# Kernel optimization log

Measured on AMD Instinct MI355X. Metric: run time of the kernel, lower is better.

## Reference

```python
import jax, jax.numpy as jnp
import numpy as np

T, B, D, H = 64, 512, 512, 2048


def setup_inputs() -> dict:
    key = jax.random.key(0)
    ks = jax.random.split(key, 6)
    y0 = jax.random.normal(ks[0], (B, D), dtype=jnp.float32)
    # strictly increasing per-sample time grids with small dt for stability
    dt = jax.random.uniform(ks[1], (T, B), dtype=jnp.float32) * 0.01 + 0.001
    t = jnp.cumsum(dt, axis=0)
    W1 = jax.random.normal(ks[2], (D, H), dtype=jnp.float32) * (1.0 / np.sqrt(D))
    b1 = jnp.zeros((H,), dtype=jnp.float32)
    W2 = jax.random.normal(ks[3], (H, D), dtype=jnp.float32) * (1.0 / np.sqrt(H))
    b2 = jnp.zeros((D,), dtype=jnp.float32)
    return {"y0": y0, "t": t, "W1": W1, "b1": b1, "W2": W2, "b2": b2}


def reference(y0, t, W1, b1, W2, b2):
    # func(t, y): autonomous 2-layer tanh MLP (t unused, as in common NeuralODE funcs)
    def f(y):
        return jnp.tanh(y @ W1 + b1) @ W2 + b2

    def step(y, dt):  # y: [B, D], dt: [B]
        dtb = dt[:, None]
        k1 = dtb * f(y)
        k2 = dtb * f(y + k1 * 0.5)
        k3 = dtb * f(y + k2 * 0.5)
        k4 = dtb * f(y + k3)
        y_new = y + (k1 + 2.0 * k2 + 2.0 * k3 + k4) / 6.0
        return y_new, y_new

    dts = t[1:] - t[:-1]  # [T-1, B] per-sample step sizes
    _, ys = jax.lax.scan(step, y0, dts)
    return jnp.concatenate([y0[None], ys], axis=0)  # [T, B, D]
```

## Files before the change

kernel.cpp:

```cpp
#include <hip/hip_runtime.h>

#define Tn 64
#define Bn 512
#define Dn 512
#define Hn 2048

typedef __attribute__((ext_vector_type(8))) short s16x8;
typedef __attribute__((ext_vector_type(4))) float f32x4;
typedef __attribute__((ext_vector_type(4))) unsigned int u32x4;
typedef unsigned int u32;
typedef unsigned long long u64;
typedef unsigned short u16;

__device__ __forceinline__ u16 f2bf(float f) {
    u32 u = __builtin_bit_cast(u32, f);
    return (u16)((u + 0x7fffu + ((u >> 16) & 1u)) >> 16);
}
__device__ __forceinline__ float bf2f(u32 v) {
    return __builtin_bit_cast(float, v << 16);
}
__device__ __forceinline__ float tanh_fast(float x) {
    float e = __builtin_amdgcn_exp2f(x * 2.885390081777927f);
    return 1.0f - 2.0f * __builtin_amdgcn_rcpf(e + 1.0f);
}
__device__ __forceinline__ u32 agent_ld(const u32* p) {
    return __hip_atomic_load((u32*)p, __ATOMIC_RELAXED, __HIP_MEMORY_SCOPE_AGENT);
}
__device__ __forceinline__ void agent_st(u32* p, u32 v) {
    __hip_atomic_store(p, v, __ATOMIC_RELAXED, __HIP_MEMORY_SCOPE_AGENT);
}
__device__ __forceinline__ u32 get_xcc() {
    u32 x;
    asm volatile("s_getreg_b32 %0, hwreg(HW_REG_XCC_ID)" : "=s"(x));
    return x & 0xffu;
}

template<bool XL>
__device__ __forceinline__ void eld128(u32x4& d, u32 vo, const void* base) {
    if constexpr (XL)
        asm volatile("global_load_dwordx4 %0, %1, %2 sc0"
                     : "=v"(d) : "v"(vo), "s"(base) : "memory");
    else
        asm volatile("global_load_dwordx4 %0, %1, %2 sc0 sc1 nt"
                     : "=v"(d) : "v"(vo), "s"(base) : "memory");
}
template<bool XL>
__device__ __forceinline__ void eld32(u32& d, u32 vo, const void* base) {
    if constexpr (XL)
        asm volatile("global_load_dword %0, %1, %2 sc0"
                     : "=v"(d) : "v"(vo), "s"(base) : "memory");
    else
        asm volatile("global_load_dword %0, %1, %2 sc0 sc1 nt"
                     : "=v"(d) : "v"(vo), "s"(base) : "memory");
}
template<bool XL>
__device__ __forceinline__ void est64(void* pa, u64 v) {
    if constexpr (XL)
        asm volatile("global_store_dwordx2 %0, %1, off sc0" :: "v"(pa), "v"(v) : "memory");
    else
        asm volatile("global_store_dwordx2 %0, %1, off sc0 sc1" :: "v"(pa), "v"(v) : "memory");
}
template<bool XL>
__device__ __forceinline__ void est32(void* pa, u32 v) {
    if constexpr (XL)
        asm volatile("global_store_dword %0, %1, off sc0" :: "v"(pa), "v"(v) : "memory");
    else
        asm volatile("global_store_dword %0, %1, off sc0 sc1" :: "v"(pa), "v"(v) : "memory");
}

__global__ void pack_w(const float* __restrict__ W1, const float* __restrict__ W2,
                       u16* __restrict__ w1p, u16* __restrict__ w2p) {
    const int i = blockIdx.x * 256 + threadIdx.x;
    const int e = i & 7;
    const int lane = (i >> 3) & 63;
    const int krem = ((lane >> 4) << 3) + e;
    const int ncol = lane & 15;
    {
        const int kt = (i >> 9) & 15, nt = i >> 13;
        const int k = (kt << 5) + krem, n = (nt << 4) + ncol;
        w1p[i] = f2bf(W1[k * Hn + n]);
    }
    {
        const int kt = (i >> 9) & 63, nt = i >> 15;
        const int k = (kt << 5) + krem, n = (nt << 4) + ncol;
        w2p[i] = f2bf(W2[k * Dn + n]);
    }
}


template<bool XL>
__device__ __forceinline__ void stage_a(const u32* ybrC, char* ldsA, int tid) {
    u32x4 d0, d1;
    const u32 vo = (u32)(tid << 5);
    eld128<XL>(d0, vo, ybrC);
    eld128<XL>(d1, vo + 16u, ybrC);
    asm volatile("s_waitcnt vmcnt(0)" : "+v"(d0), "+v"(d1) :: "memory");
    const u32 row = (u32)(tid >> 5);
    const u32 dst = vo ^ ((row & 7u) << 4);
    *(u32x4*)(ldsA + dst) = d0;
    *(u32x4*)(ldsA + (dst ^ 16u)) = d1;
}

__device__ __forceinline__ void stage_a0(const float* y0, int c, char* ldsA, int tid) {
    const float4* yc = (const float4*)(y0 + (size_t)(c << 4) * Dn);
    #pragma unroll
    for (int it = 0; it < 4; ++it) {
        const int idx = (it << 9) + tid;
        const float4 v = yc[idx];
        const u32 row = (u32)idx >> 7;
        u64 pk = (u64)((u32)f2bf(v.x) | ((u32)f2bf(v.y) << 16)) |
                 ((u64)((u32)f2bf(v.z) | ((u32)f2bf(v.w) << 16)) << 32);
        const u32 dst = (row * 1024u + ((u32)(idx & 127) << 3)) ^ ((row & 7u) << 4);
        *(u64*)(ldsA + dst) = pk;
    }
}

__device__ __forceinline__ void gemm1(const char* ldsA, char* ldsH,
                                      const s16x8 (&w1r)[16], float bia,
                                      u32 abase, u32 aswz, int w, int l15, int kg) {
    f32x4 g1 = f32x4{bia, bia, bia, bia};
    #pragma unroll
    for (int kt = 0; kt < 16; ++kt) {
        const s16x8 a = *(const s16x8*)(ldsA + ((abase + ((u32)kt << 6)) ^ aswz));
        g1 = __builtin_amdgcn_mfma_f32_16x16x32_bf16(a, w1r[kt], g1, 0, 0, 0);
    }
    #pragma unroll
    for (int j = 0; j < 4; ++j) {
        const u32 row = (u32)((kg << 2) + j);
        const u32 bo = (row * 256u + (((u32)(w << 4) + (u32)l15) << 1)) ^ ((row & 7u) << 4);
        *(u16*)(ldsH + bo) = f2bf(tanh_fast(g1[j]));
    }
}

template<bool XL>
__device__ __forceinline__ void gemm2_store(const char* ldsH, char* kpC,
                                            const s16x8 (&w2r)[4][4],
                                            u32 hbase, u32 aswz, int w, int l15,
                                            int kg, int h) {
    f32x4 acc[4];
    #pragma unroll
    for (int c = 0; c < 4; ++c) acc[c] = f32x4{0.f, 0.f, 0.f, 0.f};
    #pragma unroll
    for (int ks2 = 0; ks2 < 4; ++ks2) {
        const s16x8 ha = *(const s16x8*)(ldsH + ((hbase + ((u32)ks2 << 6)) ^ aswz));
        #pragma unroll
        for (int c = 0; c < 4; ++c)
            acc[c] = __builtin_amdgcn_mfma_f32_16x16x32_bf16(ha, w2r[c][ks2], acc[c], 0, 0, 0);
    }
    #pragma unroll
    for (int c = 0; c < 4; ++c) {
        const int nt = (w << 2) + c;
        const int o = nt >> 1;
        const int sc2 = ((nt & 1) << 4) + l15;
        u64 pk = (u64)((u32)f2bf(acc[c][0]) | ((u32)f2bf(acc[c][1]) << 16)) |
                 ((u64)((u32)f2bf(acc[c][2]) | ((u32)f2bf(acc[c][3]) << 16)) << 32);
        void* pa = kpC + (size_t)((o << 4) + h) * 1024 + (u32)((sc2 << 5) + (kg << 3));
        est64<XL>(pa, pk);
    }
}

template<bool XL>
__device__ __forceinline__ void owner_phase(int s, float& ys, float& ks, float& dtv,
                                            int brow, const char* kpC, u32* ybrC,
                                            const float* tt, float* out, float b2c,
                                            int colg, int sc, int rm, int h, int tid) {
    float sacc = 0.f;
    {
        const u32 bo = ((u32)h << 14) + (u32)((sc << 5) + ((rm >> 1) << 2));
        u32 t0,t1,t2,t3,t4,t5,t6,t7,t8,t9,ta,tb,tc,td,te,tf;
        eld32<XL>(t0, bo + (0u << 10), kpC);  eld32<XL>(t1, bo + (1u << 10), kpC);
        eld32<XL>(t2, bo + (2u << 10), kpC);  eld32<XL>(t3, bo + (3u << 10), kpC);
        eld32<XL>(t4, bo + (4u << 10), kpC);  eld32<XL>(t5, bo + (5u << 10), kpC);
        eld32<XL>(t6, bo + (6u << 10), kpC);  eld32<XL>(t7, bo + (7u << 10), kpC);
        eld32<XL>(t8, bo + (8u << 10), kpC);  eld32<XL>(t9, bo + (9u << 10), kpC);
        eld32<XL>(ta, bo + (10u << 10), kpC); eld32<XL>(tb, bo + (11u << 10), kpC);
        eld32<XL>(tc, bo + (12u << 10), kpC); eld32<XL>(td, bo + (13u << 10), kpC);
        eld32<XL>(te, bo + (14u << 10), kpC); eld32<XL>(tf, bo + (15u << 10), kpC);
        asm volatile("s_waitcnt vmcnt(0)"
                     : "+v"(t0),"+v"(t1),"+v"(t2),"+v"(t3),
                       "+v"(t4),"+v"(t5),"+v"(t6),"+v"(t7),
                       "+v"(t8),"+v"(t9),"+v"(ta),"+v"(tb),
                       "+v"(tc),"+v"(td),"+v"(te),"+v"(tf) :: "memory");
        const bool hi = (rm & 1);
#define ACC1(d) sacc += bf2f(hi ? ((d) >> 16) : ((d) & 0xffffu))
        ACC1(t0); ACC1(t1); ACC1(t2); ACC1(t3);
        ACC1(t4); ACC1(t5); ACC1(t6); ACC1(t7);
        ACC1(t8); ACC1(t9); ACC1(ta); ACC1(tb);
        ACC1(tc); ACC1(td); ACC1(te); ACC1(tf);
#undef ACC1
    }
    const int step = s >> 2, sub = s & 3;
    if (sub == 0)
        dtv = tt[(step + 1) * Bn + brow] - tt[step * Bn + brow];
    const float kk = dtv * (sacc + b2c);
    float yin;
    if (sub == 0)      { ks = kk;         yin = ys + 0.5f * kk; }
    else if (sub == 1) { ks += 2.f * kk;  yin = ys + 0.5f * kk; }
    else if (sub == 2) { ks += 2.f * kk;  yin = ys + kk; }
    else {
        ks += kk; ys += ks * (1.f / 6.f); yin = ys;
        __builtin_nontemporal_store(ys, &out[((step + 1) * Bn + brow) * Dn + colg]);
    }
    if (s < 251) {
        const u32 my = (u32)f2bf(yin);
        const u32 pu = (u32)__shfl_xor((int)my, 16, 64);
        if ((sc & 1) == 0) {
            u32* ba = ybrC + (rm << 8) + (h << 4) + (sc >> 1);
            est32<XL>(ba, my | (pu << 16));
        }
    }
}

template<bool XL>
__device__ __forceinline__ void ode_loop(
    const float* y0, const float* tt, float* out,
    char* A0, char* A1, char* H0, char* H1,
    const s16x8 (&w1r)[16], const s16x8 (&w2r)[4][4],
    float bia, float b2c, u32 abase, u32 aswz, u32 hbase,
    u32* ybr0, u32* ybr1, char* kp0, char* kp1,
    u32* fl1c0, u32* fl1c1, u32* fl2c0, u32* fl2c1,
    int c0, int c1, int brow0, int brow1, int colg,
    int tid, int w, int l15, int kg, int sc, int rm, int h,
    float ys0, float ys1) {
    float ks0 = 0.f, ks1 = 0.f, dt0 = 0.f, dt1 = 0.f;
    #pragma unroll 1
    for (int s = 0; s < 252; ++s) {
        if (s == 0) {
            stage_a0(y0, c0, A0, tid);
            stage_a0(y0, c1, A1, tid);
        } else {
            if (tid < 32) {
                u32* f = (tid < 16) ? (fl2c0 + tid) : (fl2c1 + (tid & 15));
                while (agent_ld(f) < (u32)s) __builtin_amdgcn_s_sleep(1);
            }
            __syncthreads();
            stage_a<XL>(ybr0, A0, tid);
            stage_a<XL>(ybr1, A1, tid);
        }
        __syncthreads();
        gemm1(A0, H0, w1r, bia, abase, aswz, w, l15, kg);
        gemm1(A1, H1, w1r, bia, abase, aswz, w, l15, kg);
        __syncthreads();
        gemm2_store<XL>(H0, kp0, w2r, hbase, aswz, w, l15, kg, h);
        gemm2_store<XL>(H1, kp1, w2r, hbase, aswz, w, l15, kg, h);
        asm volatile("s_waitcnt vmcnt(0)" ::: "memory");
        __syncthreads();
        if (tid == 0) {
            agent_st(fl1c0 + h, (u32)(s + 1));
            agent_st(fl1c1 + h, (u32)(s + 1));
        }
        if (tid < 32) {
            u32* f = (tid < 16) ? (fl1c0 + tid) : (fl1c1 + (tid & 15));
            while (agent_ld(f) < (u32)(s + 1)) __builtin_amdgcn_s_sleep(1);
        }
        __syncthreads();
        owner_phase<XL>(s, ys0, ks0, dt0, brow0, kp0, ybr0,
                        tt, out, b2c, colg, sc, rm, h, tid);
        owner_phase<XL>(s, ys1, ks1, dt1, brow1, kp1, ybr1,
                        tt, out, b2c, colg, sc, rm, h, tid);
        if (s < 251) {
            asm volatile("s_waitcnt vmcnt(0)" ::: "memory");
            __syncthreads();
            if (tid == 0) {
                agent_st(fl2c0 + h, (u32)(s + 1));
                agent_st(fl2c1 + h, (u32)(s + 1));
            }
        }
    }
}

__launch_bounds__(512, 2)
__global__ void ode_v12(const float* __restrict__ y0, const float* __restrict__ tt,
                        const float* __restrict__ b1, const float* __restrict__ b2,
                        const u16* __restrict__ w1p, const u16* __restrict__ w2p,
                        float* __restrict__ out, u16* __restrict__ ybuf,
                        u16* __restrict__ kpart, u32* __restrict__ flags1,
                        u32* __restrict__ flags2, u32* __restrict__ xslot,
                        u32* __restrict__ xmode) {
    __shared__ u16 lds_A0[16 * 512], lds_A1[16 * 512];
    __shared__ u16 lds_H0[16 * 128], lds_H1[16 * 128];
    __shared__ u32 smode;
    char* A0 = (char*)lds_A0; char* A1 = (char*)lds_A1;
    char* H0 = (char*)lds_H0; char* H1 = (char*)lds_H1;

    const int tid = threadIdx.x;
    const int w = tid >> 6, lane = tid & 63, l15 = lane & 15, kg = lane >> 4;
    const int p = blockIdx.x & 15, h = blockIdx.x >> 4;
    const int c0 = p << 1, c1 = c0 + 1;

    if (tid == 0) {
        agent_st(xslot + (p << 4) + h, get_xcc() + 1u);
        if (h == 0) {
            u32 ref = 0; bool same = true;
            #pragma unroll 1
            for (int i = 0; i < 16; ++i) {
                u32 v;
                while ((v = agent_ld(xslot + (p << 4) + i)) == 0u)
                    __builtin_amdgcn_s_sleep(1);
                if (i == 0) ref = v; else same = same && (v == ref);
            }
            agent_st(xmode + p, same ? 1u : 2u);
        }
        u32 m;
        while ((m = agent_ld(xmode + p)) == 0u) __builtin_amdgcn_s_sleep(1);
        smode = m;
    }

    const int sc = tid >> 4, rm = tid & 15;
    const int colg = (h << 5) + sc;
    const int brow0 = (c0 << 4) + rm, brow1 = (c1 << 4) + rm;
    const float b2c = b2[colg];
    float ys0 = y0[brow0 * Dn + colg];
    float ys1 = y0[brow1 * Dn + colg];
    __builtin_nontemporal_store(ys0, &out[brow0 * Dn + colg]);
    __builtin_nontemporal_store(ys1, &out[brow1 * Dn + colg]);

    s16x8 w1r[16];
    #pragma unroll
    for (int kt = 0; kt < 16; ++kt)
        w1r[kt] = *(const s16x8*)&w1p[((size_t)((h << 3) + w) * 16 + kt) * 512 + (lane << 3)];
    s16x8 w2r[4][4];
    #pragma unroll
    for (int cc = 0; cc < 4; ++cc)
        #pragma unroll
        for (int ks2 = 0; ks2 < 4; ++ks2)
            w2r[cc][ks2] = *(const s16x8*)&w2p[((size_t)((w << 2) + cc) * 64 + (h << 2) + ks2) * 512 + (lane << 3)];
    const float bia = b1[(h << 7) + (w << 4) + l15];

    const u32 abase = (u32)l15 * 1024u + ((u32)kg << 4);
    const u32 aswz = ((u32)(l15 & 7)) << 4;
    const u32 hbase = (u32)l15 * 256u + ((u32)kg << 4);

    u32* ybr0 = (u32*)(ybuf + (size_t)c0 * 16 * 512);
    u32* ybr1 = (u32*)(ybuf + (size_t)c1 * 16 * 512);
    char* kp0 = (char*)kpart + (size_t)c0 * (256 * 1024);
    char* kp1 = (char*)kpart + (size_t)c1 * (256 * 1024);
    u32* fl1c0 = flags1 + (c0 << 4); u32* fl1c1 = flags1 + (c1 << 4);
    u32* fl2c0 = flags2 + (c0 << 4); u32* fl2c1 = flags2 + (c1 << 4);

    __syncthreads();
    const u32 mode = smode;

    if (mode == 1u)
        ode_loop<true>(y0, tt, out, A0, A1, H0, H1, w1r, w2r, bia, b2c,
                       abase, aswz, hbase, ybr0, ybr1, kp0, kp1,
                       fl1c0, fl1c1, fl2c0, fl2c1, c0, c1, brow0, brow1, colg,
                       tid, w, l15, kg, sc, rm, h, ys0, ys1);
    else
        ode_loop<false>(y0, tt, out, A0, A1, H0, H1, w1r, w2r, bia, b2c,
                        abase, aswz, hbase, ybr0, ybr1, kp0, kp1,
                        fl1c0, fl1c1, fl2c0, fl2c1, c0, c1, brow0, brow1, colg,
                        tid, w, l15, kg, sc, rm, h, ys0, ys1);
}

__launch_bounds__(512, 2)
__global__ void ode_rk4_fb(const float* __restrict__ y0, const float* __restrict__ tt,
                           const float* __restrict__ b1, const float* __restrict__ b2,
                           const u16* __restrict__ w1p, const u16* __restrict__ w2p,
                           float* __restrict__ out) {
    __shared__ u16 lds_ys[16 * Dn];
    __shared__ u16 lds_hid[16 * Hn];
    __shared__ float lds_dt[16];
    const int tid = threadIdx.x;
    const int w = tid >> 6, lane = tid & 63, l15 = lane & 15, kgrp = lane >> 4;
    const int row0 = blockIdx.x << 4;
    float yreg[4][4], ksum[4][4], kk[4][4];
    float b1v[16], b2v[4], dtv[4];
    #pragma unroll
    for (int nt = 0; nt < 16; ++nt) b1v[nt] = b1[(w << 8) + (nt << 4) + l15];
    #pragma unroll
    for (int c = 0; c < 4; ++c) b2v[c] = b2[(w << 6) + (c << 4) + l15];
    #pragma unroll
    for (int c = 0; c < 4; ++c)
        #pragma unroll
        for (int j = 0; j < 4; ++j) {
            const int rr = (kgrp << 2) + j;
            const int col = (w << 6) + (c << 4) + l15;
            const float v = y0[(row0 + rr) * Dn + col];
            yreg[c][j] = v; ksum[c][j] = 0.f; kk[c][j] = 0.f;
            out[(row0 + rr) * Dn + col] = v;
        }
    const u16* wv1 = w1p + ((w << 4) * (16 * 512)) + (lane << 3);
    const u16* wv2 = w2p + ((w << 2) * (64 * 512)) + (lane << 3);
    const int arow = l15;
    const unsigned swzA = (unsigned)((arow & 7) << 3);
    for (int step = 0; step < Tn - 1; ++step) {
        if (tid < 16)
            lds_dt[tid] = tt[(step + 1) * Bn + row0 + tid] - tt[step * Bn + row0 + tid];
        #pragma unroll 1
        for (int s = 0; s < 4; ++s) {
            const float ci = (s == 3) ? 1.0f : ((s == 0) ? 0.0f : 0.5f);
            #pragma unroll
            for (int c = 0; c < 4; ++c)
                #pragma unroll
                for (int j = 0; j < 4; ++j) {
                    const int rr = (kgrp << 2) + j;
                    const int col = (w << 6) + (c << 4) + l15;
                    lds_ys[(unsigned)((rr << 9) + col) ^ (unsigned)((rr & 7) << 3)] =
                        f2bf(yreg[c][j] + ci * kk[c][j]);
                }
            __syncthreads();
            if (s == 0) {
                #pragma unroll
                for (int j = 0; j < 4; ++j) dtv[j] = lds_dt[(kgrp << 2) + j];
            }
            f32x4 acc[16];
            #pragma unroll
            for (int nt = 0; nt < 16; ++nt)
                #pragma unroll
                for (int j = 0; j < 4; ++j) acc[nt][j] = b1v[nt];
            #pragma unroll 2
            for (int kt = 0; kt < 16; ++kt) {
                const unsigned ia = ((unsigned)((arow << 9) + (kt << 5) + (kgrp << 3))) ^ swzA;
                const s16x8 a = *(const s16x8*)&lds_ys[ia];
                #pragma unroll
                for (int nt = 0; nt < 16; ++nt) {
                    const s16x8 bfrag = *(const s16x8*)&wv1[nt * 8192 + kt * 512];
                    acc[nt] = __builtin_amdgcn_mfma_f32_16x16x32_bf16(a, bfrag, acc[nt], 0, 0, 0);
                }
            }
            #pragma unroll
            for (int nt = 0; nt < 16; ++nt)
                #pragma unroll
                for (int j = 0; j < 4; ++j) {
                    const int rr = (kgrp << 2) + j;
                    const int col = (w << 8) + (nt << 4) + l15;
                    lds_hid[(unsigned)((rr << 11) + col) ^ (unsigned)((rr & 7) << 3)] =
                        f2bf(tanh_fast(acc[nt][j]));
                }
            __syncthreads();
            f32x4 acc2[4];
            #pragma unroll
            for (int c = 0; c < 4; ++c)
                #pragma unroll
                for (int j = 0; j < 4; ++j) acc2[c][j] = 0.f;
            #pragma unroll 2
            for (int kt = 0; kt < 64; ++kt) {
                const unsigned ia = ((unsigned)((arow << 11) + (kt << 5) + (kgrp << 3))) ^ swzA;
                const s16x8 a = *(const s16x8*)&lds_hid[ia];
                #pragma unroll
                for (int c = 0; c < 4; ++c) {
                    const s16x8 bfrag = *(const s16x8*)&wv2[c * 32768 + kt * 512];
                    acc2[c] = __builtin_amdgcn_mfma_f32_16x16x32_bf16(a, bfrag, acc2[c], 0, 0, 0);
                }
            }
            const float wq = (s == 0 || s == 3) ? 1.0f : 2.0f;
            #pragma unroll
            for (int c = 0; c < 4; ++c)
                #pragma unroll
                for (int j = 0; j < 4; ++j) {
                    const float kv = dtv[j] * (acc2[c][j] + b2v[c]);
                    kk[c][j] = kv;
                    ksum[c][j] = (s == 0) ? kv : ksum[c][j] + wq * kv;
                }
        }
        #pragma unroll
        for (int c = 0; c < 4; ++c)
            #pragma unroll
            for (int j = 0; j < 4; ++j) {
                const int rr = (kgrp << 2) + j;
                const int col = (w << 6) + (c << 4) + l15;
                yreg[c][j] += ksum[c][j] * (1.0f / 6.0f);
                out[((step + 1) * Bn + row0 + rr) * Dn + col] = yreg[c][j];
            }
    }
}

extern "C" void kernel_launch(void* const* d_in, const int* in_sizes, int n_in,
                              void* d_out, int out_size, void* d_ws, size_t ws_size,
                              hipStream_t stream) {
    const float* y0 = (const float*)d_in[0];
    const float* tt = (const float*)d_in[1];
    const float* W1 = (const float*)d_in[2];
    const float* b1 = (const float*)d_in[3];
    const float* W2 = (const float*)d_in[4];
    const float* b2 = (const float*)d_in[5];
    float* out = (float*)d_out;
    char* ws = (char*)d_ws;

    const size_t sz_fl = (size_t)64 * 1024;
    const size_t sz_x = 4096;
    const size_t sz_w = (size_t)Dn * Hn * 2;
    const size_t sz_ybuf = (size_t)32 * 16 * 512 * 2;
    const size_t sz_kpart = (size_t)32 * 16 * 16 * 1024;
    const size_t needed = 2 * sz_fl + sz_x + 2 * sz_w + sz_ybuf + sz_kpart + 4096;

    u32* flags1 = (u32*)ws;
    u32* flags2 = (u32*)(ws + sz_fl);
    u32* xslot = (u32*)(ws + 2 * sz_fl);
    u32* xmode = (u32*)(ws + 2 * sz_fl + 1024);
    u16* w1p = (u16*)(ws + 2 * sz_fl + sz_x);
    u16* w2p = (u16*)(ws + 2 * sz_fl + sz_x + sz_w);
    u16* ybuf = (u16*)(ws + 2 * sz_fl + sz_x + 2 * sz_w);
    u16* kpart = (u16*)(ws + 2 * sz_fl + sz_x + 2 * sz_w + sz_ybuf);

    if (ws_size >= needed) {
        hipMemsetAsync(ws, 0, 2 * sz_fl + sz_x, stream);
        pack_w<<<4096, 256, 0, stream>>>(W1, W2, w1p, w2p);
        void* args[] = {&y0, &tt, &b1, &b2, &w1p, &w2p, &out, &ybuf, &kpart,
                        &flags1, &flags2, &xslot, &xmode};
        hipLaunchCooperativeKernel((void*)ode_v12, dim3(256), dim3(512), args, 0, stream);
    } else {
        u16* f1 = (u16*)ws;
        u16* f2 = f1 + (size_t)Dn * Hn;
        pack_w<<<4096, 256, 0, stream>>>(W1, W2, f1, f2);
        ode_rk4_fb<<<32, 512, 0, stream>>>(y0, tt, b1, b2, f1, f2, out);
    }
}
```

Baseline: 1.859 ms.

## Repartition cooperative RK4 kernel: one batch chunk per block, 8 hidden-slice blocks

The cooperative ODE kernel changes from 16 chunk-pairs × 16 hidden-slice blocks to 32 chunks × 8 hidden-slice blocks. Each block now handles a single 16-row batch chunk with double the W1/W2 register slice, so each group synchronizes across 8 blocks instead of 16. This is meant to shrink the per-substep flag fan-in and the partial-sum reduction, which now reads 8 partials instead of 16. In exchange each block holds twice the weight registers, so launch bounds drop to 1 block per CU and register pressure rises.

```diff
diff --git a/kernel.cpp b/kernel.cpp
--- a/kernel.cpp
+++ b/kernel.cpp
@@ -36,22 +36,22 @@
 }
 
 template<bool XL>
-__device__ __forceinline__ void eld128(u32x4& d, u32 vo, const void* base) {
+__device__ __forceinline__ void eld128p(u32x4& d, const void* p) {
     if constexpr (XL)
-        asm volatile("global_load_dwordx4 %0, %1, %2 sc0"
-                     : "=v"(d) : "v"(vo), "s"(base) : "memory");
+        asm volatile("global_load_dwordx4 %0, %1, off sc0"
+                     : "=v"(d) : "v"(p) : "memory");
     else
-        asm volatile("global_load_dwordx4 %0, %1, %2 sc0 sc1 nt"
-                     : "=v"(d) : "v"(vo), "s"(base) : "memory");
-}
-template<bool XL>
-__device__ __forceinline__ void eld32(u32& d, u32 vo, const void* base) {
+        asm volatile("global_load_dwordx4 %0, %1, off sc0 sc1 nt"
+                     : "=v"(d) : "v"(p) : "memory");
+}
+template<bool XL>
+__device__ __forceinline__ void eld32p(u32& d, const void* p) {
     if constexpr (XL)
-        asm volatile("global_load_dword %0, %1, %2 sc0"
-                     : "=v"(d) : "v"(vo), "s"(base) : "memory");
+        asm volatile("global_load_dword %0, %1, off sc0"
+                     : "=v"(d) : "v"(p) : "memory");
     else
-        asm volatile("global_load_dword %0, %1, %2 sc0 sc1 nt"
-                     : "=v"(d) : "v"(vo), "s"(base) : "memory");
+        asm volatile("global_load_dword %0, %1, off sc0 sc1 nt"
+                     : "=v"(d) : "v"(p) : "memory");
 }
 template<bool XL>
 __device__ __forceinline__ void est64(void* pa, u64 v) {
@@ -89,12 +89,13 @@
 
 
 template<bool XL>
-__device__ __forceinline__ void stage_a(const u32* ybrC, char* ldsA, int tid) {
+__device__ __forceinline__ void stage_a(const char* ybrC, char* ldsA, int tid) {
     u32x4 d0, d1;
+    const char* src = ybrC + ((u32)tid << 5);
+    eld128p<XL>(d0, src);
+    eld128p<XL>(d1, src + 16);
+    asm volatile("s_waitcnt vmcnt(0)" : "+v"(d0), "+v"(d1) :: "memory");
     const u32 vo = (u32)(tid << 5);
-    eld128<XL>(d0, vo, ybrC);
-    eld128<XL>(d1, vo + 16u, ybrC);
-    asm volatile("s_waitcnt vmcnt(0)" : "+v"(d0), "+v"(d1) :: "memory");
     const u32 row = (u32)(tid >> 5);
     const u32 dst = vo ^ ((row & 7u) << 4);
     *(u32x4*)(ldsA + dst) = d0;
@@ -115,242 +116,226 @@
     }
 }
 
-__device__ __forceinline__ void gemm1(const char* ldsA, char* ldsH,
-                                      const s16x8 (&w1r)[16], float bia,
-                                      u32 abase, u32 aswz, int w, int l15, int kg) {
-    f32x4 g1 = f32x4{bia, bia, bia, bia};
-    #pragma unroll
-    for (int kt = 0; kt < 16; ++kt) {
-        const s16x8 a = *(const s16x8*)(ldsA + ((abase + ((u32)kt << 6)) ^ aswz));
-        g1 = __builtin_amdgcn_mfma_f32_16x16x32_bf16(a, w1r[kt], g1, 0, 0, 0);
-    }
-    #pragma unroll
-    for (int j = 0; j < 4; ++j) {
-        const u32 row = (u32)((kg << 2) + j);
-        const u32 bo = (row * 256u + (((u32)(w << 4) + (u32)l15) << 1)) ^ ((row & 7u) << 4);
-        *(u16*)(ldsH + bo) = f2bf(tanh_fast(g1[j]));
-    }
-}
-
-template<bool XL>
-__device__ __forceinline__ void gemm2_store(const char* ldsH, char* kpC,
-                                            const s16x8 (&w2r)[4][4],
-                                            u32 hbase, u32 aswz, int w, int l15,
-                                            int kg, int h) {
-    f32x4 acc[4];
-    #pragma unroll
-    for (int c = 0; c < 4; ++c) acc[c] = f32x4{0.f, 0.f, 0.f, 0.f};
-    #pragma unroll
-    for (int ks2 = 0; ks2 < 4; ++ks2) {
-        const s16x8 ha = *(const s16x8*)(ldsH + ((hbase + ((u32)ks2 << 6)) ^ aswz));
-        #pragma unroll
-        for (int c = 0; c < 4; ++c)
-            acc[c] = __builtin_amdgcn_mfma_f32_16x16x32_bf16(ha, w2r[c][ks2], acc[c], 0, 0, 0);
-    }
-    #pragma unroll
-    for (int c = 0; c < 4; ++c) {
-        const int nt = (w << 2) + c;
-        const int o = nt >> 1;
-        const int sc2 = ((nt & 1) << 4) + l15;
-        u64 pk = (u64)((u32)f2bf(acc[c][0]) | ((u32)f2bf(acc[c][1]) << 16)) |
-                 ((u64)((u32)f2bf(acc[c][2]) | ((u32)f2bf(acc[c][3]) << 16)) << 32);
-        void* pa = kpC + (size_t)((o << 4) + h) * 1024 + (u32)((sc2 << 5) + (kg << 3));
-        est64<XL>(pa, pk);
-    }
-}
-
-template<bool XL>
-__device__ __forceinline__ void owner_phase(int s, float& ys, float& ks, float& dtv,
-                                            int brow, const char* kpC, u32* ybrC,
-                                            const float* tt, float* out, float b2c,
-                                            int colg, int sc, int rm, int h, int tid) {
-    float sacc = 0.f;
-    {
-        const u32 bo = ((u32)h << 14) + (u32)((sc << 5) + ((rm >> 1) << 2));
-        u32 t0,t1,t2,t3,t4,t5,t6,t7,t8,t9,ta,tb,tc,td,te,tf;
-        eld32<XL>(t0, bo + (0u << 10), kpC);  eld32<XL>(t1, bo + (1u << 10), kpC);
-        eld32<XL>(t2, bo + (2u << 10), kpC);  eld32<XL>(t3, bo + (3u << 10), kpC);
-        eld32<XL>(t4, bo + (4u << 10), kpC);  eld32<XL>(t5, bo + (5u << 10), kpC);
-        eld32<XL>(t6, bo + (6u << 10), kpC);  eld32<XL>(t7, bo + (7u << 10), kpC);
-        eld32<XL>(t8, bo + (8u << 10), kpC);  eld32<XL>(t9, bo + (9u << 10), kpC);
-        eld32<XL>(ta, bo + (10u << 10), kpC); eld32<XL>(tb, bo + (11u << 10), kpC);
-        eld32<XL>(tc, bo + (12u << 10), kpC); eld32<XL>(td, bo + (13u << 10), kpC);
-        eld32<XL>(te, bo + (14u << 10), kpC); eld32<XL>(tf, bo + (15u << 10), kpC);
-        asm volatile("s_waitcnt vmcnt(0)"
-                     : "+v"(t0),"+v"(t1),"+v"(t2),"+v"(t3),
-                       "+v"(t4),"+v"(t5),"+v"(t6),"+v"(t7),
-                       "+v"(t8),"+v"(t9),"+v"(ta),"+v"(tb),
-                       "+v"(tc),"+v"(td),"+v"(te),"+v"(tf) :: "memory");
-        const bool hi = (rm & 1);
-#define ACC1(d) sacc += bf2f(hi ? ((d) >> 16) : ((d) & 0xffffu))
-        ACC1(t0); ACC1(t1); ACC1(t2); ACC1(t3);
-        ACC1(t4); ACC1(t5); ACC1(t6); ACC1(t7);
-        ACC1(t8); ACC1(t9); ACC1(ta); ACC1(tb);
-        ACC1(tc); ACC1(td); ACC1(te); ACC1(tf);
-#undef ACC1
-    }
-    const int step = s >> 2, sub = s & 3;
-    if (sub == 0)
-        dtv = tt[(step + 1) * Bn + brow] - tt[step * Bn + brow];
-    const float kk = dtv * (sacc + b2c);
-    float yin;
-    if (sub == 0)      { ks = kk;         yin = ys + 0.5f * kk; }
-    else if (sub == 1) { ks += 2.f * kk;  yin = ys + 0.5f * kk; }
-    else if (sub == 2) { ks += 2.f * kk;  yin = ys + kk; }
-    else {
-        ks += kk; ys += ks * (1.f / 6.f); yin = ys;
-        __builtin_nontemporal_store(ys, &out[((step + 1) * Bn + brow) * Dn + colg]);
-    }
-    if (s < 251) {
-        const u32 my = (u32)f2bf(yin);
-        const u32 pu = (u32)__shfl_xor((int)my, 16, 64);
-        if ((sc & 1) == 0) {
-            u32* ba = ybrC + (rm << 8) + (h << 4) + (sc >> 1);
-            est32<XL>(ba, my | (pu << 16));
-        }
-    }
-}
-
 template<bool XL>
 __device__ __forceinline__ void ode_loop(
     const float* y0, const float* tt, float* out,
-    char* A0, char* A1, char* H0, char* H1,
-    const s16x8 (&w1r)[16], const s16x8 (&w2r)[4][4],
-    float bia, float b2c, u32 abase, u32 aswz, u32 hbase,
-    u32* ybr0, u32* ybr1, char* kp0, char* kp1,
-    u32* fl1c0, u32* fl1c1, u32* fl2c0, u32* fl2c1,
-    int c0, int c1, int brow0, int brow1, int colg,
-    int tid, int w, int l15, int kg, int sc, int rm, int h,
+    char* A, char* Hb,
+    const s16x8 (&w1r)[2][16], const s16x8 (&w2r)[4][8],
+    float bia0, float bia1, float b2c,
+    u32 abase, u32 aswz, u32 hbase,
+    char* ybr, char* kpc, u32* fl1, u32* fl2,
+    int c, int brow0, int brow1, int colg,
+    int tid, int w, int l15, int kg, int sc, int rp, int h,
     float ys0, float ys1) {
     float ks0 = 0.f, ks1 = 0.f, dt0 = 0.f, dt1 = 0.f;
     #pragma unroll 1
     for (int s = 0; s < 252; ++s) {
         if (s == 0) {
-            stage_a0(y0, c0, A0, tid);
-            stage_a0(y0, c1, A1, tid);
+            stage_a0(y0, c, A, tid);
         } else {
-            if (tid < 32) {
-                u32* f = (tid < 16) ? (fl2c0 + tid) : (fl2c1 + (tid & 15));
-                while (agent_ld(f) < (u32)s) __builtin_amdgcn_s_sleep(1);
+            if (tid < 8) {
+                while (agent_ld(fl2 + tid) < (u32)s) __builtin_amdgcn_s_sleep(1);
             }
             __syncthreads();
-            stage_a<XL>(ybr0, A0, tid);
-            stage_a<XL>(ybr1, A1, tid);
+            stage_a<XL>(ybr, A, tid);
         }
         __syncthreads();
-        gemm1(A0, H0, w1r, bia, abase, aswz, w, l15, kg);
-        gemm1(A1, H1, w1r, bia, abase, aswz, w, l15, kg);
+
+        {
+            f32x4 a1[2];
+            a1[0] = f32x4{bia0, bia0, bia0, bia0};
+            a1[1] = f32x4{bia1, bia1, bia1, bia1};
+            #pragma unroll
+            for (int kt = 0; kt < 16; ++kt) {
+                const s16x8 a = *(const s16x8*)(A + ((abase + ((u32)kt << 6)) ^ aswz));
+                a1[0] = __builtin_amdgcn_mfma_f32_16x16x32_bf16(a, w1r[0][kt], a1[0], 0, 0, 0);
+                a1[1] = __builtin_amdgcn_mfma_f32_16x16x32_bf16(a, w1r[1][kt], a1[1], 0, 0, 0);
+            }
+            #pragma unroll
+            for (int n = 0; n < 2; ++n) {
+                #pragma unroll
+                for (int j = 0; j < 4; ++j) {
+                    const u32 row = (u32)((kg << 2) + j);
+                    const u32 col = (u32)(((w << 1) + n) * 16 + l15);
+                    const u32 bo = (row * 512u + (col << 1)) ^ ((row & 7u) << 4);
+                    *(u16*)(Hb + bo) = f2bf(tanh_fast(a1[n][j]));
+                }
+            }
+        }
         __syncthreads();
-        gemm2_store<XL>(H0, kp0, w2r, hbase, aswz, w, l15, kg, h);
-        gemm2_store<XL>(H1, kp1, w2r, hbase, aswz, w, l15, kg, h);
+
+        {
+            f32x4 acc[4];
+            #pragma unroll
+            for (int cc = 0; cc < 4; ++cc) acc[cc] = f32x4{0.f, 0.f, 0.f, 0.f};
+            #pragma unroll
+            for (int ks = 0; ks < 8; ++ks) {
+                const s16x8 ha = *(const s16x8*)(Hb + ((hbase + ((u32)ks << 6)) ^ aswz));
+                #pragma unroll
+                for (int cc = 0; cc < 4; ++cc)
+                    acc[cc] = __builtin_amdgcn_mfma_f32_16x16x32_bf16(ha, w2r[cc][ks], acc[cc], 0, 0, 0);
+            }
+            #pragma unroll
+            for (int cc = 0; cc < 4; ++cc) {
+                const int nt = (w << 2) + cc;
+                const int o = nt >> 2;
+                const int sc2 = ((nt & 3) << 4) + l15;
+                u64 pk = (u64)((u32)f2bf(acc[cc][0]) | ((u32)f2bf(acc[cc][1]) << 16)) |
+                         ((u64)((u32)f2bf(acc[cc][2]) | ((u32)f2bf(acc[cc][3]) << 16)) << 32);
+                void* pa = kpc + (size_t)((o << 3) + h) * 2048 + (u32)((sc2 << 5) + (kg << 3));
+                est64<XL>(pa, pk);
+            }
+        }
         asm volatile("s_waitcnt vmcnt(0)" ::: "memory");
         __syncthreads();
-        if (tid == 0) {
-            agent_st(fl1c0 + h, (u32)(s + 1));
-            agent_st(fl1c1 + h, (u32)(s + 1));
-        }
-        if (tid < 32) {
-            u32* f = (tid < 16) ? (fl1c0 + tid) : (fl1c1 + (tid & 15));
-            while (agent_ld(f) < (u32)(s + 1)) __builtin_amdgcn_s_sleep(1);
+        if (tid == 0) agent_st(fl1 + h, (u32)(s + 1));
+
+        if (tid < 8) {
+            while (agent_ld(fl1 + tid) < (u32)(s + 1)) __builtin_amdgcn_s_sleep(1);
         }
         __syncthreads();
-        owner_phase<XL>(s, ys0, ks0, dt0, brow0, kp0, ybr0,
-                        tt, out, b2c, colg, sc, rm, h, tid);
-        owner_phase<XL>(s, ys1, ks1, dt1, brow1, kp1, ybr1,
-                        tt, out, b2c, colg, sc, rm, h, tid);
+
+        float s0 = 0.f, s1 = 0.f;
+        {
+            const char* kb = kpc + (size_t)((h << 3) * 2048) + (u32)((sc << 5) + (rp << 2));
+            u32 t0, t1, t2, t3, t4, t5, t6, t7;
+            eld32p<XL>(t0, kb + 0 * 2048);  eld32p<XL>(t1, kb + 1 * 2048);
+            eld32p<XL>(t2, kb + 2 * 2048);  eld32p<XL>(t3, kb + 3 * 2048);
+            eld32p<XL>(t4, kb + 4 * 2048);  eld32p<XL>(t5, kb + 5 * 2048);
+            eld32p<XL>(t6, kb + 6 * 2048);  eld32p<XL>(t7, kb + 7 * 2048);
+            asm volatile("s_waitcnt vmcnt(0)"
+                         : "+v"(t0), "+v"(t1), "+v"(t2), "+v"(t3),
+                           "+v"(t4), "+v"(t5), "+v"(t6), "+v"(t7) :: "memory");
+            s0 = bf2f(t0 & 0xffffu) + bf2f(t1 & 0xffffu) + bf2f(t2 & 0xffffu) +
+                 bf2f(t3 & 0xffffu) + bf2f(t4 & 0xffffu) + bf2f(t5 & 0xffffu) +
+                 bf2f(t6 & 0xffffu) + bf2f(t7 & 0xffffu);
+            s1 = bf2f(t0 >> 16) + bf2f(t1 >> 16) + bf2f(t2 >> 16) +
+                 bf2f(t3 >> 16) + bf2f(t4 >> 16) + bf2f(t5 >> 16) +
+                 bf2f(t6 >> 16) + bf2f(t7 >> 16);
+        }
+        const int step = s >> 2, sub = s & 3;
+        if (sub == 0) {
+            dt0 = tt[(step + 1) * Bn + brow0] - tt[step * Bn + brow0];
+            dt1 = tt[(step + 1) * Bn + brow1] - tt[step * Bn + brow1];
+        }
+        const float k0 = dt0 * (s0 + b2c), k1 = dt1 * (s1 + b2c);
+        float yin0, yin1;
+        if (sub == 0)      { ks0 = k0;        ks1 = k1;        yin0 = ys0 + 0.5f * k0; yin1 = ys1 + 0.5f * k1; }
+        else if (sub == 1) { ks0 += 2.f * k0; ks1 += 2.f * k1; yin0 = ys0 + 0.5f * k0; yin1 = ys1 + 0.5f * k1; }
+        else if (sub == 2) { ks0 += 2.f * k0; ks1 += 2.f * k1; yin0 = ys0 + k0;        yin1 = ys1 + k1; }
+        else {
+            ks0 += k0; ks1 += k1;
+            ys0 += ks0 * (1.f / 6.f); ys1 += ks1 * (1.f / 6.f);
+            yin0 = ys0; yin1 = ys1;
+            __builtin_nontemporal_store(ys0, &out[((step + 1) * Bn + brow0) * Dn + colg]);
+            __builtin_nontemporal_store(ys1, &out[((step + 1) * Bn + brow1) * Dn + colg]);
+        }
         if (s < 251) {
+            const u32 my0 = (u32)f2bf(yin0);
+            const u32 my1 = (u32)f2bf(yin1);
+            const u32 pu0 = (u32)__shfl_xor((int)my0, 8, 64);
+            const u32 pu1 = (u32)__shfl_xor((int)my1, 8, 64);
+            if ((sc & 1) == 0) {
+                const u32 w0 = my0 | (pu0 << 16);
+                const u32 w1 = my1 | (pu1 << 16);
+                void* ba0 = ybr + (size_t)(((2 * rp) << 8) + (colg >> 1)) * 4;
+                void* ba1 = ybr + (size_t)(((2 * rp + 1) << 8) + (colg >> 1)) * 4;
+                est32<XL>(ba0, w0);
+                est32<XL>(ba1, w1);
+            }
             asm volatile("s_waitcnt vmcnt(0)" ::: "memory");
             __syncthreads();
-            if (tid == 0) {
-                agent_st(fl2c0 + h, (u32)(s + 1));
-                agent_st(fl2c1 + h, (u32)(s + 1));
-            }
-        }
-    }
-}
-
-__launch_bounds__(512, 2)
-__global__ void ode_v12(const float* __restrict__ y0, const float* __restrict__ tt,
+            if (tid == 0) agent_st(fl2 + h, (u32)(s + 1));
+        }
+    }
+}
+
+__launch_bounds__(512, 1)
+__global__ void ode_v16(const float* __restrict__ y0, const float* __restrict__ tt,
                         const float* __restrict__ b1, const float* __restrict__ b2,
                         const u16* __restrict__ w1p, const u16* __restrict__ w2p,
                         float* __restrict__ out, u16* __restrict__ ybuf,
                         u16* __restrict__ kpart, u32* __restrict__ flags1,
                         u32* __restrict__ flags2, u32* __restrict__ xslot,
                         u32* __restrict__ xmode) {
-    __shared__ u16 lds_A0[16 * 512], lds_A1[16 * 512];
-    __shared__ u16 lds_H0[16 * 128], lds_H1[16 * 128];
+    __shared__ u16 lds_A[16 * 512];
+    __shared__ u16 lds_H[16 * 256];
     __shared__ u32 smode;
-    char* A0 = (char*)lds_A0; char* A1 = (char*)lds_A1;
-    char* H0 = (char*)lds_H0; char* H1 = (char*)lds_H1;
+    char* A = (char*)lds_A;
+    char* Hb = (char*)lds_H;
 
     const int tid = threadIdx.x;
     const int w = tid >> 6, lane = tid & 63, l15 = lane & 15, kg = lane >> 4;
-    const int p = blockIdx.x & 15, h = blockIdx.x >> 4;
-    const int c0 = p << 1, c1 = c0 + 1;
+    const int g = blockIdx.x & 31, h = blockIdx.x >> 5;
+    const int c = g;
 
     if (tid == 0) {
-        agent_st(xslot + (p << 4) + h, get_xcc() + 1u);
+        agent_st(xslot + (g << 3) + h, get_xcc() + 1u);
         if (h == 0) {
             u32 ref = 0; bool same = true;
             #pragma unroll 1
-            for (int i = 0; i < 16; ++i) {
+            for (int i = 0; i < 8; ++i) {
                 u32 v;
-                while ((v = agent_ld(xslot + (p << 4) + i)) == 0u)
+                while ((v = agent_ld(xslot + (g << 3) + i)) == 0u)
                     __builtin_amdgcn_s_sleep(1);
                 if (i == 0) ref = v; else same = same && (v == ref);
             }
-            agent_st(xmode + p, same ? 1u : 2u);
+            agent_st(xmode + g, same ? 1u : 2u);
         }
         u32 m;
-        while ((m = agent_ld(xmode + p)) == 0u) __builtin_amdgcn_s_sleep(1);
+        while ((m = agent_ld(xmode + g)) == 0u) __builtin_amdgcn_s_sleep(1);
         smode = m;
     }
 
-    const int sc = tid >> 4, rm = tid & 15;
-    const int colg = (h << 5) + sc;
-    const int brow0 = (c0 << 4) + rm, brow1 = (c1 << 4) + rm;
+    const int sc = tid >> 3;
+    const int rp = tid & 7;
+    const int colg = (h << 6) + sc;
+    const int brow0 = (c << 4) + 2 * rp, brow1 = brow0 + 1;
     const float b2c = b2[colg];
     float ys0 = y0[brow0 * Dn + colg];
     float ys1 = y0[brow1 * Dn + colg];
     __builtin_nontemporal_store(ys0, &out[brow0 * Dn + colg]);
     __builtin_nontemporal_store(ys1, &out[brow1 * Dn + colg]);
 
-    s16x8 w1r[16];
-    #pragma unroll
-    for (int kt = 0; kt < 16; ++kt)
-        w1r[kt] = *(const s16x8*)&w1p[((size_t)((h << 3) + w) * 16 + kt) * 512 + (lane << 3)];
-    s16x8 w2r[4][4];
-    #pragma unroll
-    for (int cc = 0; cc < 4; ++cc)
+    s16x8 w1r[2][16];
+    #pragma unroll
+    for (int n = 0; n < 2; ++n) {
+        const int nt1 = (h << 4) + (w << 1) + n;
         #pragma unroll
-        for (int ks2 = 0; ks2 < 4; ++ks2)
-            w2r[cc][ks2] = *(const s16x8*)&w2p[((size_t)((w << 2) + cc) * 64 + (h << 2) + ks2) * 512 + (lane << 3)];
-    const float bia = b1[(h << 7) + (w << 4) + l15];
+        for (int kt = 0; kt < 16; ++kt)
+            w1r[n][kt] = *(const s16x8*)&w1p[((size_t)nt1 * 16 + kt) * 512 + (lane << 3)];
+    }
+    s16x8 w2r[4][8];
+    #pragma unroll
+    for (int cc = 0; cc < 4; ++cc) {
+        const int nt2 = (w << 2) + cc;
+        #pragma unroll
+        for (int ks = 0; ks < 8; ++ks)
+            w2r[cc][ks] = *(const s16x8*)&w2p[((size_t)nt2 * 64 + (h << 3) + ks) * 512 + (lane << 3)];
+    }
+    const float bia0 = b1[(h << 8) + (w << 5) + l15];
+    const float bia1 = b1[(h << 8) + (w << 5) + 16 + l15];
 
     const u32 abase = (u32)l15 * 1024u + ((u32)kg << 4);
     const u32 aswz = ((u32)(l15 & 7)) << 4;
-    const u32 hbase = (u32)l15 * 256u + ((u32)kg << 4);
-
-    u32* ybr0 = (u32*)(ybuf + (size_t)c0 * 16 * 512);
-    u32* ybr1 = (u32*)(ybuf + (size_t)c1 * 16 * 512);
-    char* kp0 = (char*)kpart + (size_t)c0 * (256 * 1024);
-    char* kp1 = (char*)kpart + (size_t)c1 * (256 * 1024);
-    u32* fl1c0 = flags1 + (c0 << 4); u32* fl1c1 = flags1 + (c1 << 4);
-    u32* fl2c0 = flags2 + (c0 << 4); u32* fl2c1 = flags2 + (c1 << 4);
+    const u32 hbase = (u32)l15 * 512u + ((u32)kg << 4);
+
+    char* ybr = (char*)(ybuf + (size_t)c * 16 * 512);
+    char* kpc = (char*)kpart + (size_t)c * 131072;
+    u32* fl1 = flags1 + (c << 4);
+    u32* fl2 = flags2 + (c << 4);
 
     __syncthreads();
     const u32 mode = smode;
 
     if (mode == 1u)
-        ode_loop<true>(y0, tt, out, A0, A1, H0, H1, w1r, w2r, bia, b2c,
-                       abase, aswz, hbase, ybr0, ybr1, kp0, kp1,
-                       fl1c0, fl1c1, fl2c0, fl2c1, c0, c1, brow0, brow1, colg,
-                       tid, w, l15, kg, sc, rm, h, ys0, ys1);
+        ode_loop<true>(y0, tt, out, A, Hb, w1r, w2r, bia0, bia1, b2c,
+                       abase, aswz, hbase, ybr, kpc, fl1, fl2,
+                       c, brow0, brow1, colg, tid, w, l15, kg, sc, rp, h, ys0, ys1);
     else
-        ode_loop<false>(y0, tt, out, A0, A1, H0, H1, w1r, w2r, bia, b2c,
-                        abase, aswz, hbase, ybr0, ybr1, kp0, kp1,
-                        fl1c0, fl1c1, fl2c0, fl2c1, c0, c1, brow0, brow1, colg,
-                        tid, w, l15, kg, sc, rm, h, ys0, ys1);
+        ode_loop<false>(y0, tt, out, A, Hb, w1r, w2r, bia0, bia1, b2c,
+                        abase, aswz, hbase, ybr, kpc, fl1, fl2,
+                        c, brow0, brow1, colg, tid, w, l15, kg, sc, rp, h, ys0, ys1);
 }
 
 __launch_bounds__(512, 2)
@@ -482,7 +467,7 @@
     const size_t sz_x = 4096;
     const size_t sz_w = (size_t)Dn * Hn * 2;
     const size_t sz_ybuf = (size_t)32 * 16 * 512 * 2;
-    const size_t sz_kpart = (size_t)32 * 16 * 16 * 1024;
+    const size_t sz_kpart = (size_t)32 * 131072;
     const size_t needed = 2 * sz_fl + sz_x + 2 * sz_w + sz_ybuf + sz_kpart + 4096;
 
     u32* flags1 = (u32*)ws;
@@ -499,7 +484,7 @@
         pack_w<<<4096, 256, 0, stream>>>(W1, W2, w1p, w2p);
         void* args[] = {&y0, &tt, &b1, &b2, &w1p, &w2p, &out, &ybuf, &kpart,
                         &flags1, &flags2, &xslot, &xmode};
-        hipLaunchCooperativeKernel((void*)ode_v12, dim3(256), dim3(512), args, 0, stream);
+        hipLaunchCooperativeKernel((void*)ode_v16, dim3(256), dim3(512), args, 0, stream);
     } else {
         u16* f1 = (u16*)ws;
         u16* f2 = f1 + (size_t)Dn * Hn;
```

New measurement: 4.004 ms. 115% more time.
